# Optimization experiments

Hardware: AMD Instinct MI355X
Metric: run time of the kernel (lower is better)

Reference implementation:

```python
import jax, jax.numpy as jnp
import numpy as np

B, T, E = 2, 2048, 1024
H = 8
DV = 2048  # value_dim
DK = E // H   # 128
DH = DV // H  # 256
EPS = 1e-6


def _make_decay_mask(h, t):
    gammas = 1.0 - 2.0 ** (-5.0 - np.arange(h, dtype=np.float64))
    idx = np.arange(t)
    diff = idx[:, None] - idx[None, :]
    exp = np.where(diff >= 0, diff, 0)
    mask = (gammas[:, None, None] ** exp[None]) * (diff >= 0)[None]
    # RetNet normalizes the decay mask row-wise by sqrt of row sum
    mask = mask / np.sqrt(mask.sum(-1, keepdims=True))
    return np.nan_to_num(mask).astype(np.float32)


def setup_inputs() -> dict:
    key = jax.random.key(0)
    ks = jax.random.split(key, 8)
    hidden_states = jax.random.normal(ks[0], (B, T, E), dtype=jnp.float32)
    # xpos-style angles for sin/cos over key_dim (pairs share an angle)
    pos = np.arange(T, dtype=np.float32)[:, None]
    inv_freq = 1.0 / (10000.0 ** (np.arange(0, DK, 2, dtype=np.float32) / DK))
    angle = pos * inv_freq[None, :]              # [T, DK/2]
    angle = np.repeat(angle, 2, axis=-1)         # [T, DK]
    sin = jnp.asarray(np.sin(angle))
    cos = jnp.asarray(np.cos(angle))
    decay_mask = jnp.asarray(_make_decay_mask(H, T))
    s = 0.02
    Wq = jax.random.normal(ks[1], (E, E), dtype=jnp.float32) * s
    Wk = jax.random.normal(ks[2], (E, E), dtype=jnp.float32) * s
    Wv = jax.random.normal(ks[3], (DV, E), dtype=jnp.float32) * s
    Wg = jax.random.normal(ks[4], (DV, E), dtype=jnp.float32) * s
    Wo = jax.random.normal(ks[5], (E, DV), dtype=jnp.float32) * s
    return {"hidden_states": hidden_states, "sin": sin, "cos": cos,
            "decay_mask": decay_mask, "Wq": Wq, "Wk": Wk, "Wv": Wv,
            "Wg": Wg, "Wo": Wo}


def rotate_every_two(x):
    x1 = x[..., ::2]
    x2 = x[..., 1::2]
    return jnp.stack((-x2, x1), axis=-1).reshape(x.shape)


def theta_shift(x, sin, cos):
    return x * cos + rotate_every_two(x) * sin


def reference(hidden_states, sin, cos, decay_mask, Wq, Wk, Wv, Wg, Wo):
    b, t, e = hidden_states.shape
    scaling = DK ** -0.5
    q = jnp.einsum('bti,oi->bto', hidden_states, Wq)
    k = jnp.einsum('bti,oi->bto', hidden_states, Wk)
    v = jnp.einsum('bti,oi->bto', hidden_states, Wv)
    g = jnp.einsum('bti,oi->bto', hidden_states, Wg)
    # split heads -> [B, H, T, d]
    q = q.reshape(b, t, H, DK).transpose(0, 2, 1, 3)
    k = k.reshape(b, t, H, DK).transpose(0, 2, 1, 3) * scaling
    v = v.reshape(b, t, H, DH).transpose(0, 2, 1, 3)
    qr = theta_shift(q, sin, cos)   # sin/cos [T, DK] broadcast
    kr = theta_shift(k, sin, cos)
    # parallel retention
    retention = jnp.einsum('bhtd,bhsd->bhts', qr, kr) * decay_mask[None]
    denom = jnp.clip(jnp.abs(retention.sum(-1, keepdims=True)), 1.0, 5e4)
    retention = retention / jax.lax.stop_gradient(denom)
    out = jnp.einsum('bhts,bhsd->bhtd', retention, v)  # [B,H,T,DH]
    # per-head RMS group norm (no affine)
    out = out * jax.lax.rsqrt(jnp.mean(out * out, axis=-1, keepdims=True) + EPS)
    out = out.transpose(0, 2, 1, 3).reshape(b, t, DV)
    out = jax.nn.silu(g) * out
    return jnp.einsum('btv,ev->bte', out, Wo)
```

## Files before the change

### kernel.cpp

```cpp
#include <hip/hip_runtime.h>
#include <hip/hip_bf16.h>
#include <stdint.h>

#define BB 2
#define TT 2048
#define EE 1024
#define HH 8
#define DKC 128
#define DHC 256
#define DVC 2048
#define MM (BB*TT)

typedef __attribute__((ext_vector_type(8))) short bf16x8;
typedef __attribute__((ext_vector_type(4))) float f32x4;

__device__ __forceinline__ unsigned short f2b(float f) {
    __hip_bfloat16 h = __float2bfloat16(f);
    return __builtin_bit_cast(unsigned short, h);
}

__device__ __forceinline__ void gl_lds16(const void* g, void* lds) {
    __builtin_amdgcn_global_load_lds(
        (const __attribute__((address_space(1))) void*)g,
        (__attribute__((address_space(3))) void*)lds, 16, 0, 0);
}

__global__ void cvt_kernel(const float* __restrict__ src, unsigned short* __restrict__ dst, int n) {
    int i = (blockIdx.x * blockDim.x + threadIdx.x) * 4;
    if (i >= n) return;
    float4 v = *reinterpret_cast<const float4*>(src + i);
    ushort4 o;
    o.x = f2b(v.x); o.y = f2b(v.y); o.z = f2b(v.z); o.w = f2b(v.w);
    *reinterpret_cast<ushort4*>(dst + i) = o;
}

template<int K>
__global__ __launch_bounds__(256) void gemm_bt(const unsigned short* __restrict__ A,
                                               const unsigned short* __restrict__ Bm,
                                               float* __restrict__ C, int N) {
    __shared__ unsigned short lA[128*32];
    __shared__ unsigned short lB[128*32];
    const int t = threadIdx.x;
    const int w = t >> 6, l = t & 63;
    const int m0 = blockIdx.y * 128, n0 = blockIdx.x * 128;
    const int wm = (w >> 1) * 64, wn = (w & 1) * 64;
    f32x4 acc[4][4] = {};

    const int srow = w*16 + (l >> 2);
    const int scol = (l & 3) * 8;
    const unsigned short* Abase = A + (long)(m0 + srow) * K + scol;
    const unsigned short* Bbase = Bm + (long)(n0 + srow) * K + scol;
    char* ldsA = (char*)lA;
    char* ldsB = (char*)lB;

    for (int kk = 0; kk < K; kk += 32) {
        __syncthreads();
        gl_lds16(Abase + kk,          ldsA + w*1024);
        gl_lds16(Abase + 64*K + kk,   ldsA + 4096 + w*1024);
        gl_lds16(Bbase + kk,          ldsB + w*1024);
        gl_lds16(Bbase + 64*K + kk,   ldsB + 4096 + w*1024);
        __syncthreads();
        bf16x8 a[4], b[4];
        #pragma unroll
        for (int i = 0; i < 4; i++)
            a[i] = *reinterpret_cast<const bf16x8*>(&lA[(wm + i*16 + (l&15))*32 + (l>>4)*8]);
        #pragma unroll
        for (int i = 0; i < 4; i++)
            b[i] = *reinterpret_cast<const bf16x8*>(&lB[(wn + i*16 + (l&15))*32 + (l>>4)*8]);
        #pragma unroll
        for (int mi = 0; mi < 4; mi++)
            #pragma unroll
            for (int ni = 0; ni < 4; ni++)
                acc[mi][ni] = __builtin_amdgcn_mfma_f32_16x16x32_bf16(a[mi], b[ni], acc[mi][ni], 0, 0, 0);
    }
    const int cr = (l >> 4) * 4, cc = l & 15;
    #pragma unroll
    for (int mi = 0; mi < 4; mi++)
        #pragma unroll
        for (int ni = 0; ni < 4; ni++) {
            float* cp = C + (long)(m0 + wm + mi*16 + cr) * N + (n0 + wn + ni*16 + cc);
            #pragma unroll
            for (int j = 0; j < 4; j++) cp[(long)j * N] = acc[mi][ni][j];
        }
}

__global__ void rope_kernel(const float* __restrict__ qkvg,
                            const float* __restrict__ sinp, const float* __restrict__ cosp,
                            unsigned short* __restrict__ qr, unsigned short* __restrict__ kr) {
    const float scaling = 0.08838834764831845f;
    int gid = blockIdx.x * 256 + threadIdx.x;
    int m  = gid >> 9;
    int pe = gid & 511;
    int c  = pe * 2;
    int h  = c >> 7, d = c & 127;
    int b  = m >> 11, tt = m & 2047;
    float s1 = sinp[tt*128 + d], c1 = cosp[tt*128 + d];
    const float* row = qkvg + (long)m * 6144;
    float q1 = row[c], q2 = row[c+1];
    float k1 = row[1024 + c] * scaling, k2 = row[1024 + c + 1] * scaling;
    long o = ((long)(b*HH + h) * TT + tt) * DKC + d;
    unsigned int qw = (unsigned int)f2b(q1*c1 - q2*s1) | ((unsigned int)f2b(q2*c1 + q1*s1) << 16);
    unsigned int kw = (unsigned int)f2b(k1*c1 - k2*s1) | ((unsigned int)f2b(k2*c1 + k1*s1) << 16);
    *(unsigned int*)(qr + o) = qw;
    *(unsigned int*)(kr + o) = kw;
}

__global__ __launch_bounds__(256) void vtrans_kernel(const float* __restrict__ qkvg, unsigned short* __restrict__ vt) {
    __shared__ float tile[32][33];
    int bh = blockIdx.z;
    int b = bh >> 3, h = bh & 7;
    int t0 = blockIdx.x * 32, d0 = blockIdx.y * 32;
    int tx = threadIdx.x & 31, ty = threadIdx.x >> 5;
    #pragma unroll
    for (int r = 0; r < 4; r++) {
        int trow = t0 + ty + r*8;
        tile[ty + r*8][tx] = qkvg[((long)(b*TT + trow)) * 6144 + 2048 + h*256 + d0 + tx];
    }
    __syncthreads();
    #pragma unroll
    for (int r = 0; r < 4; r++) {
        int d = d0 + ty + r*8;
        vt[((long)(bh*256 + d)) * TT + t0 + tx] = f2b(tile[tx][ty + r*8]);
    }
}

__global__ __launch_bounds__(256) void retention_kernel(
        const unsigned short* __restrict__ qr, const unsigned short* __restrict__ kr,
        const unsigned short* __restrict__ vt,
        const float* __restrict__ qkvg, unsigned short* __restrict__ gated) {
    __shared__ unsigned short lK[64*128];
    __shared__ unsigned short lV[256*64];
    __shared__ unsigned short lS[64*64];
    __shared__ float lDen[64];
    __shared__ float lSsq[4][64];

    const int t = threadIdx.x, w = t >> 6, l = t & 63;
    const int g = l >> 4, c = l & 15;
    const int blk = blockIdx.x;
    const int bh = blk & 15;
    const int qq = blk >> 4;
    const int ttile = (qq < 16) ? qq : (47 - qq);
    const int b = bh >> 3, h = bh & 7;
    const int t0 = ttile * 64;
    const int tw = w * 16;
    const int dq = w * 64;

    const float gamma = 1.0f - exp2f(-(float)(5 + h));
    const float l2g   = log2f(gamma);
    const float ig    = exp2f((float)(5 + h));
    float rnorm[4];
    #pragma unroll
    for (int j = 0; j < 4; j++) {
        int tg = t0 + tw + g*4 + j;
        rnorm[j] = rsqrtf((1.0f - exp2f((float)(tg + 1) * l2g)) * ig);
    }

    bf16x8 qf[4];
    {
        const unsigned short* qrow = qr + ((long)bh * TT + t0 + tw + c) * DKC + g*8;
        #pragma unroll
        for (int ks = 0; ks < 4; ks++)
            qf[ks] = *reinterpret_cast<const bf16x8*>(qrow + ks*32);
    }

    f32x4 acc[4][4] = {};
    float rsum[4] = {0.f, 0.f, 0.f, 0.f};

    for (int sb = 0; sb <= ttile; sb++) {
        const int s0 = sb * 64;
        __syncthreads();
        #pragma unroll
        for (int r = 0; r < 4; r++) {
            int row = r*16 + w*4 + g;
            int gb = ((l & 15)*16) ^ ((row & 15) << 4);
            gl_lds16(kr + ((long)bh*TT + s0 + row)*DKC + (gb >> 1), (char*)lK + r*4096 + w*1024);
        }
        #pragma unroll
        for (int r = 0; r < 8; r++) {
            int d = r*32 + w*8 + (l >> 3);
            int gb = ((l & 7)*16) ^ ((d & 7) << 4);
            gl_lds16(vt + ((long)bh*DHC + d)*TT + s0 + (gb >> 1), (char*)lV + r*4096 + w*1024);
        }
        __syncthreads();

        f32x4 sf[4] = {};
        #pragma unroll
        for (int ks = 0; ks < 4; ks++) {
            #pragma unroll
            for (int ni = 0; ni < 4; ni++) {
                int row = ni*16 + c;
                int cb = (ks*64 + g*16) ^ ((row & 15) << 4);
                bf16x8 kf = *reinterpret_cast<const bf16x8*>((const char*)lK + row*256 + cb);
                sf[ni] = __builtin_amdgcn_mfma_f32_16x16x32_bf16(qf[ks], kf, sf[ni], 0, 0, 0);
            }
        }
        #pragma unroll
        for (int ni = 0; ni < 4; ni++) {
            #pragma unroll
            for (int j = 0; j < 4; j++) {
                int rloc = tw + g*4 + j;
                int e = (t0 + rloc) - (s0 + ni*16 + c);
                float dv = (e >= 0) ? exp2f((float)e * l2g) * rnorm[j] : 0.0f;
                float sv = sf[ni][j] * dv;
                rsum[j] += sv;
                int scol = ni*16 + c;
                int cb2 = (scol*2) ^ ((rloc & 7) << 4);
                *(unsigned short*)((char*)lS + rloc*128 + cb2) = f2b(sv);
            }
        }
        __syncthreads();

        #pragma unroll
        for (int ks = 0; ks < 2; ks++) {
            bf16x8 af[4];
            #pragma unroll
            for (int mi = 0; mi < 4; mi++) {
                int r2 = mi*16 + c;
                int cb = (ks*64 + g*16) ^ ((r2 & 7) << 4);
                af[mi] = *reinterpret_cast<const bf16x8*>((const char*)lS + r2*128 + cb);
            }
            #pragma unroll
            for (int ni = 0; ni < 4; ni++) {
                int d = dq + ni*16 + c;
                int cb = (ks*64 + g*16) ^ ((d & 7) << 4);
                bf16x8 vf = *reinterpret_cast<const bf16x8*>((const char*)lV + d*128 + cb);
                #pragma unroll
                for (int mi = 0; mi < 4; mi++)
                    acc[mi][ni] = __builtin_amdgcn_mfma_f32_16x16x32_bf16(af[mi], vf, acc[mi][ni], 0, 0, 0);
            }
        }
    }

    #pragma unroll
    for (int j = 0; j < 4; j++) {
        float v = rsum[j];
        v += __shfl_xor(v, 1); v += __shfl_xor(v, 2); v += __shfl_xor(v, 4); v += __shfl_xor(v, 8);
        if (c == 0) lDen[tw + g*4 + j] = fminf(fmaxf(fabsf(v), 1.0f), 50000.0f);
    }
    __syncthreads();

    #pragma unroll
    for (int mi = 0; mi < 4; mi++) {
        #pragma unroll
        for (int j = 0; j < 4; j++) {
            int rloc = mi*16 + g*4 + j;
            float den = lDen[rloc];
            float ss = 0.f;
            #pragma unroll
            for (int ni = 0; ni < 4; ni++) {
                float o = acc[mi][ni][j] / den;
                acc[mi][ni][j] = o;
                ss += o*o;
            }
            ss += __shfl_xor(ss, 1); ss += __shfl_xor(ss, 2); ss += __shfl_xor(ss, 4); ss += __shfl_xor(ss, 8);
            if (c == 0) lSsq[w][rloc] = ss;
        }
    }
    __syncthreads();

    #pragma unroll
    for (int mi = 0; mi < 4; mi++) {
        #pragma unroll
        for (int j = 0; j < 4; j++) {
            int rloc = mi*16 + g*4 + j;
            float ssq = lSsq[0][rloc] + lSsq[1][rloc] + lSsq[2][rloc] + lSsq[3][rloc];
            float scale = rsqrtf(ssq * (1.0f/256.0f) + 1e-6f);
            long m = (long)b*TT + t0 + rloc;
            #pragma unroll
            for (int ni = 0; ni < 4; ni++) {
                int vcol = h*256 + dq + ni*16 + c;
                float gv = qkvg[m*6144 + 4096 + vcol];
                float sg = gv / (1.0f + __expf(-gv));
                gated[m*2048 + vcol] = f2b(acc[mi][ni][j] * scale * sg);
            }
        }
    }
}

extern "C" void kernel_launch(void* const* d_in, const int* in_sizes, int n_in,
                              void* d_out, int out_size, void* d_ws, size_t ws_size,
                              hipStream_t stream) {
    const float* hs    = (const float*)d_in[0];
    const float* sinp  = (const float*)d_in[1];
    const float* cosp  = (const float*)d_in[2];
    const float* Wq    = (const float*)d_in[4];
    const float* Wk    = (const float*)d_in[5];
    const float* Wv    = (const float*)d_in[6];
    const float* Wg    = (const float*)d_in[7];
    const float* Wo    = (const float*)d_in[8];
    float* out = (float*)d_out;

    char* ws = (char*)d_ws;
    unsigned short* hsb   = (unsigned short*)(ws);
    unsigned short* Wc    = (unsigned short*)(ws + 8388608);
    unsigned short* Wob   = (unsigned short*)(ws + 20971520);
    float*          qkvg  = (float*)        (ws + 25165824);
    unsigned short* qrb   = (unsigned short*)(ws + 125829120);
    unsigned short* krb   = (unsigned short*)(ws + 134217728);
    unsigned short* vtb   = (unsigned short*)(ws + 142606336);
    unsigned short* gated = (unsigned short*)(ws + 159383552);

    cvt_kernel<<<4096, 256, 0, stream>>>(hs, hsb, 4194304);
    cvt_kernel<<<1024, 256, 0, stream>>>(Wq, Wc,           1048576);
    cvt_kernel<<<1024, 256, 0, stream>>>(Wk, Wc + 1048576, 1048576);
    cvt_kernel<<<2048, 256, 0, stream>>>(Wv, Wc + 2097152, 2097152);
    cvt_kernel<<<2048, 256, 0, stream>>>(Wg, Wc + 4194304, 2097152);
    cvt_kernel<<<2048, 256, 0, stream>>>(Wo, Wob,          2097152);

    gemm_bt<1024><<<dim3(48, 32), 256, 0, stream>>>(hsb, Wc, qkvg, 6144);
    rope_kernel<<<8192, 256, 0, stream>>>(qkvg, sinp, cosp, qrb, krb);
    vtrans_kernel<<<dim3(64, 8, 16), 256, 0, stream>>>(qkvg, vtb);
    retention_kernel<<<512, 256, 0, stream>>>(qrb, krb, vtb, qkvg, gated);
    gemm_bt<2048><<<dim3(8, 32), 256, 0, stream>>>(gated, Wob, out, 1024);
}
```

Measured before the change: 428.6 us.

## Replace QKVG projection GEMM with pipelined 256x256 kernel emitting bf16 output

Adds a new 512-thread GEMM with 256x256 tiles that prefetches K-slices straight into LDS through several stages, uses explicit waitcnt/barrier phases with raised priority around the MFMA blocks, and remaps block IDs across XCDs. The fused QKVG projection output is now stored as bf16 rather than fp32, which halves its write traffic and the later reads in rope, V-transpose and the gating epilogue. The workspace layout shrinks to match. This adds one more bf16 rounding of q/k/v/g, and the hand-written pipeline depends on exact vmcnt accounting being correct.

```diff
diff --git a/kernel.cpp b/kernel.cpp
--- a/kernel.cpp
+++ b/kernel.cpp
@@ -18,6 +18,10 @@
     __hip_bfloat16 h = __float2bfloat16(f);
     return __builtin_bit_cast(unsigned short, h);
 }
+__device__ __forceinline__ float b2f(unsigned short u) {
+    __hip_bfloat16 h = __builtin_bit_cast(__hip_bfloat16, u);
+    return __bfloat162float(h);
+}
 
 __device__ __forceinline__ void gl_lds16(const void* g, void* lds) {
     __builtin_amdgcn_global_load_lds(
@@ -32,6 +36,98 @@
     ushort4 o;
     o.x = f2b(v.x); o.y = f2b(v.y); o.z = f2b(v.z); o.w = f2b(v.w);
     *reinterpret_cast<ushort4*>(dst + i) = o;
+}
+
+template<int K>
+__global__ __launch_bounds__(512, 2) void gemm8p(const unsigned short* __restrict__ A,
+                                                 const unsigned short* __restrict__ Bm,
+                                                 unsigned short* __restrict__ C, int N, int nbx) {
+    __shared__ unsigned short lds[65536];
+    char* ldsb = (char*)lds;
+    const int tid = threadIdx.x;
+    const int w = tid >> 6, l = tid & 63;
+    const int wm = w >> 2, wn = w & 3;
+    const int q = l >> 4, r = l & 15;
+
+    int bid = blockIdx.x;
+    int cpx = gridDim.x >> 3;
+    int wg = (bid & 7) * cpx + (bid >> 3);
+    const long m0 = (long)(wg / nbx) * 256;
+    const long n0 = (long)(wg % nbx) * 256;
+
+    const int srow = tid >> 2;
+    const int scol = (tid & 3) * 8;
+    const unsigned short* Asrc = A + (m0 + srow) * K + scol;
+    const unsigned short* Bsrc = Bm + (n0 + srow) * K + scol;
+
+#define STAGE(OP, T_, KH_) do {                                                   \
+    char* dst_ = ldsb + (OP) * 65536 + (((T_) & 1) * 2 + (KH_)) * 16384 + w * 1024; \
+    const unsigned short* s_ = ((OP) ? Bsrc : Asrc) + (long)(T_) * 64 + (KH_) * 32; \
+    gl_lds16(s_, dst_);                                                           \
+    gl_lds16(s_ + 128 * K, dst_ + 8192);                                          \
+} while (0)
+
+    const int arow = (wm * 128 + r) * 64 + q * 16;
+    const int brow = (wn * 64 + r) * 64 + q * 16;
+
+    f32x4 acc[8][4] = {};
+    bf16x8 af[8];
+
+    STAGE(0, 0, 0); STAGE(1, 0, 0);
+    STAGE(0, 0, 1); STAGE(1, 0, 1);
+    STAGE(0, 1, 0); STAGE(1, 1, 0);
+    asm volatile("s_waitcnt vmcnt(8)" ::: "memory");
+    __builtin_amdgcn_s_barrier();
+
+#define PHASE(T_, KH_, NH_, SOP, ST_, SKH_, DOVM) do {                            \
+    const char* Ah_ = ldsb + (((T_) & 1) * 2 + (KH_)) * 16384;                    \
+    const char* Bh_ = ldsb + 65536 + (((T_) & 1) * 2 + (KH_)) * 16384;            \
+    if ((NH_) == 0) {                                                             \
+        _Pragma("unroll") for (int mf = 0; mf < 8; mf++)                          \
+            af[mf] = *(const bf16x8*)(Ah_ + arow + mf * 1024);                    \
+    }                                                                             \
+    bf16x8 b0 = *(const bf16x8*)(Bh_ + brow + (NH_) * 2048);                      \
+    bf16x8 b1 = *(const bf16x8*)(Bh_ + brow + (NH_) * 2048 + 1024);               \
+    STAGE(SOP, ST_, SKH_);                                                        \
+    if (DOVM) asm volatile("s_waitcnt vmcnt(8)" ::: "memory");                    \
+    __builtin_amdgcn_s_barrier();                                                 \
+    asm volatile("s_waitcnt lgkmcnt(0)" ::: "memory");                            \
+    __builtin_amdgcn_sched_barrier(0);                                            \
+    __builtin_amdgcn_s_setprio(1);                                                \
+    _Pragma("unroll") for (int mf = 0; mf < 8; mf++) {                            \
+        acc[mf][(NH_) * 2]     = __builtin_amdgcn_mfma_f32_16x16x32_bf16(af[mf], b0, acc[mf][(NH_) * 2], 0, 0, 0);     \
+        acc[mf][(NH_) * 2 + 1] = __builtin_amdgcn_mfma_f32_16x16x32_bf16(af[mf], b1, acc[mf][(NH_) * 2 + 1], 0, 0, 0); \
+    }                                                                             \
+    __builtin_amdgcn_s_setprio(0);                                                \
+    __builtin_amdgcn_s_barrier();                                                 \
+} while (0)
+
+    const int mask = (K / 64) - 1;
+    for (int t = 0; t < K / 64; t += 2) {
+        PHASE(t,     0, 0, 0, t + 1,          1, 0);
+        PHASE(t,     0, 1, 1, t + 1,          1, 1);
+        PHASE(t,     1, 0, 0, (t + 2) & mask, 0, 0);
+        PHASE(t,     1, 1, 1, (t + 2) & mask, 0, 1);
+        PHASE(t + 1, 0, 0, 0, (t + 2) & mask, 1, 0);
+        PHASE(t + 1, 0, 1, 1, (t + 2) & mask, 1, 1);
+        PHASE(t + 1, 1, 0, 0, (t + 3) & mask, 0, 0);
+        PHASE(t + 1, 1, 1, 1, (t + 3) & mask, 0, 1);
+    }
+    asm volatile("s_waitcnt vmcnt(0)" ::: "memory");
+
+    const int cr = q * 4;
+    #pragma unroll
+    for (int mf = 0; mf < 8; mf++)
+        #pragma unroll
+        for (int nf = 0; nf < 4; nf++) {
+            long crow = m0 + wm * 128 + mf * 16 + cr;
+            long ccol = n0 + wn * 64 + nf * 16 + r;
+            #pragma unroll
+            for (int j = 0; j < 4; j++)
+                C[(crow + j) * N + ccol] = f2b(acc[mf][nf][j]);
+        }
+#undef PHASE
+#undef STAGE
 }
 
 template<int K>
@@ -84,7 +180,7 @@
         }
 }
 
-__global__ void rope_kernel(const float* __restrict__ qkvg,
+__global__ void rope_kernel(const unsigned short* __restrict__ qkvg,
                             const float* __restrict__ sinp, const float* __restrict__ cosp,
                             unsigned short* __restrict__ qr, unsigned short* __restrict__ kr) {
     const float scaling = 0.08838834764831845f;
@@ -95,9 +191,9 @@
     int h  = c >> 7, d = c & 127;
     int b  = m >> 11, tt = m & 2047;
     float s1 = sinp[tt*128 + d], c1 = cosp[tt*128 + d];
-    const float* row = qkvg + (long)m * 6144;
-    float q1 = row[c], q2 = row[c+1];
-    float k1 = row[1024 + c] * scaling, k2 = row[1024 + c + 1] * scaling;
+    const unsigned short* row = qkvg + (long)m * 6144;
+    float q1 = b2f(row[c]), q2 = b2f(row[c+1]);
+    float k1 = b2f(row[1024 + c]) * scaling, k2 = b2f(row[1024 + c + 1]) * scaling;
     long o = ((long)(b*HH + h) * TT + tt) * DKC + d;
     unsigned int qw = (unsigned int)f2b(q1*c1 - q2*s1) | ((unsigned int)f2b(q2*c1 + q1*s1) << 16);
     unsigned int kw = (unsigned int)f2b(k1*c1 - k2*s1) | ((unsigned int)f2b(k2*c1 + k1*s1) << 16);
@@ -105,29 +201,29 @@
     *(unsigned int*)(kr + o) = kw;
 }
 
-__global__ __launch_bounds__(256) void vtrans_kernel(const float* __restrict__ qkvg, unsigned short* __restrict__ vt) {
-    __shared__ float tile[32][33];
+__global__ __launch_bounds__(256) void vtrans_kernel(const unsigned short* __restrict__ qkvg, unsigned short* __restrict__ vt) {
+    __shared__ unsigned short tile[32][33];
     int bh = blockIdx.z;
     int b = bh >> 3, h = bh & 7;
     int t0 = blockIdx.x * 32, d0 = blockIdx.y * 32;
     int tx = threadIdx.x & 31, ty = threadIdx.x >> 5;
     #pragma unroll
-    for (int r = 0; r < 4; r++) {
-        int trow = t0 + ty + r*8;
-        tile[ty + r*8][tx] = qkvg[((long)(b*TT + trow)) * 6144 + 2048 + h*256 + d0 + tx];
+    for (int rr = 0; rr < 4; rr++) {
+        int trow = t0 + ty + rr*8;
+        tile[ty + rr*8][tx] = qkvg[((long)(b*TT + trow)) * 6144 + 2048 + h*256 + d0 + tx];
     }
     __syncthreads();
     #pragma unroll
-    for (int r = 0; r < 4; r++) {
-        int d = d0 + ty + r*8;
-        vt[((long)(bh*256 + d)) * TT + t0 + tx] = f2b(tile[tx][ty + r*8]);
+    for (int rr = 0; rr < 4; rr++) {
+        int d = d0 + ty + rr*8;
+        vt[((long)(bh*256 + d)) * TT + t0 + tx] = tile[tx][ty + rr*8];
     }
 }
 
 __global__ __launch_bounds__(256) void retention_kernel(
         const unsigned short* __restrict__ qr, const unsigned short* __restrict__ kr,
         const unsigned short* __restrict__ vt,
-        const float* __restrict__ qkvg, unsigned short* __restrict__ gated) {
+        const unsigned short* __restrict__ qkvg, unsigned short* __restrict__ gated) {
     __shared__ unsigned short lK[64*128];
     __shared__ unsigned short lV[256*64];
     __shared__ unsigned short lS[64*64];
@@ -170,16 +266,16 @@
         const int s0 = sb * 64;
         __syncthreads();
         #pragma unroll
-        for (int r = 0; r < 4; r++) {
-            int row = r*16 + w*4 + g;
+        for (int rr = 0; rr < 4; rr++) {
+            int row = rr*16 + w*4 + g;
             int gb = ((l & 15)*16) ^ ((row & 15) << 4);
-            gl_lds16(kr + ((long)bh*TT + s0 + row)*DKC + (gb >> 1), (char*)lK + r*4096 + w*1024);
-        }
-        #pragma unroll
-        for (int r = 0; r < 8; r++) {
-            int d = r*32 + w*8 + (l >> 3);
+            gl_lds16(kr + ((long)bh*TT + s0 + row)*DKC + (gb >> 1), (char*)lK + rr*4096 + w*1024);
+        }
+        #pragma unroll
+        for (int rr = 0; rr < 8; rr++) {
+            int d = rr*32 + w*8 + (l >> 3);
             int gb = ((l & 7)*16) ^ ((d & 7) << 4);
-            gl_lds16(vt + ((long)bh*DHC + d)*TT + s0 + (gb >> 1), (char*)lV + r*4096 + w*1024);
+            gl_lds16(vt + ((long)bh*DHC + d)*TT + s0 + (gb >> 1), (char*)lV + rr*4096 + w*1024);
         }
         __syncthreads();
 
@@ -212,12 +308,12 @@
 
         #pragma unroll
         for (int ks = 0; ks < 2; ks++) {
-            bf16x8 af[4];
+            bf16x8 afr[4];
             #pragma unroll
             for (int mi = 0; mi < 4; mi++) {
                 int r2 = mi*16 + c;
                 int cb = (ks*64 + g*16) ^ ((r2 & 7) << 4);
-                af[mi] = *reinterpret_cast<const bf16x8*>((const char*)lS + r2*128 + cb);
+                afr[mi] = *reinterpret_cast<const bf16x8*>((const char*)lS + r2*128 + cb);
             }
             #pragma unroll
             for (int ni = 0; ni < 4; ni++) {
@@ -226,7 +322,7 @@
                 bf16x8 vf = *reinterpret_cast<const bf16x8*>((const char*)lV + d*128 + cb);
                 #pragma unroll
                 for (int mi = 0; mi < 4; mi++)
-                    acc[mi][ni] = __builtin_amdgcn_mfma_f32_16x16x32_bf16(af[mi], vf, acc[mi][ni], 0, 0, 0);
+                    acc[mi][ni] = __builtin_amdgcn_mfma_f32_16x16x32_bf16(afr[mi], vf, acc[mi][ni], 0, 0, 0);
             }
         }
     }
@@ -269,7 +365,7 @@
             #pragma unroll
             for (int ni = 0; ni < 4; ni++) {
                 int vcol = h*256 + dq + ni*16 + c;
-                float gv = qkvg[m*6144 + 4096 + vcol];
+                float gv = b2f(qkvg[m*6144 + 4096 + vcol]);
                 float sg = gv / (1.0f + __expf(-gv));
                 gated[m*2048 + vcol] = f2b(acc[mi][ni][j] * scale * sg);
             }
@@ -294,11 +390,11 @@
     unsigned short* hsb   = (unsigned short*)(ws);
     unsigned short* Wc    = (unsigned short*)(ws + 8388608);
     unsigned short* Wob   = (unsigned short*)(ws + 20971520);
-    float*          qkvg  = (float*)        (ws + 25165824);
-    unsigned short* qrb   = (unsigned short*)(ws + 125829120);
-    unsigned short* krb   = (unsigned short*)(ws + 134217728);
-    unsigned short* vtb   = (unsigned short*)(ws + 142606336);
-    unsigned short* gated = (unsigned short*)(ws + 159383552);
+    unsigned short* qkvgb = (unsigned short*)(ws + 25165824);
+    unsigned short* qrb   = (unsigned short*)(ws + 75497472);
+    unsigned short* krb   = (unsigned short*)(ws + 83886080);
+    unsigned short* vtb   = (unsigned short*)(ws + 92274688);
+    unsigned short* gated = (unsigned short*)(ws + 109051904);
 
     cvt_kernel<<<4096, 256, 0, stream>>>(hs, hsb, 4194304);
     cvt_kernel<<<1024, 256, 0, stream>>>(Wq, Wc,           1048576);
@@ -307,9 +403,9 @@
     cvt_kernel<<<2048, 256, 0, stream>>>(Wg, Wc + 4194304, 2097152);
     cvt_kernel<<<2048, 256, 0, stream>>>(Wo, Wob,          2097152);
 
-    gemm_bt<1024><<<dim3(48, 32), 256, 0, stream>>>(hsb, Wc, qkvg, 6144);
-    rope_kernel<<<8192, 256, 0, stream>>>(qkvg, sinp, cosp, qrb, krb);
-    vtrans_kernel<<<dim3(64, 8, 16), 256, 0, stream>>>(qkvg, vtb);
-    retention_kernel<<<512, 256, 0, stream>>>(qrb, krb, vtb, qkvg, gated);
+    gemm8p<1024><<<384, 512, 0, stream>>>(hsb, Wc, qkvgb, 6144, 24);
+    rope_kernel<<<8192, 256, 0, stream>>>(qkvgb, sinp, cosp, qrb, krb);
+    vtrans_kernel<<<dim3(64, 8, 16), 256, 0, stream>>>(qkvgb, vtb);
+    retention_kernel<<<512, 256, 0, stream>>>(qrb, krb, vtb, qkvgb, gated);
     gemm_bt<2048><<<dim3(8, 32), 256, 0, stream>>>(gated, Wob, out, 1024);
 }
```

Measured after the change: 412.1 us. -3.8%, faster.
